# Kernel tuning notes

Hardware: AMD Instinct MI355X
Metric: run time of the kernel (lower is better)

Reference implementation:

```python
import jax, jax.numpy as jnp
import numpy as np

MAX_ITER = 20
F_TOL = 1e-6
FREE_NUM = 64  # free_idx[1] + 1
TRUNC = (0, 512)  # truncate_idx


def setup_inputs() -> dict:
    key = jax.random.key(0)
    ks = jax.random.split(key, 8)
    bsz, in_dim, hid, out_dim, m = 1024, 512, 1024, 256, 128
    return {
        "b_primal": jax.random.normal(ks[0], (bsz, in_dim), jnp.float32),
        "W0": jax.random.normal(ks[1], (hid, in_dim), jnp.float32) / np.sqrt(in_dim).astype(np.float32),
        "b0": jnp.zeros((hid,), jnp.float32),
        "W1": jax.random.normal(ks[2], (hid, hid), jnp.float32) / np.sqrt(hid).astype(np.float32),
        "b1": jnp.zeros((hid,), jnp.float32),
        "W2": jax.random.normal(ks[3], (out_dim, hid), jnp.float32) / np.sqrt(hid).astype(np.float32),
        "b2": jnp.zeros((out_dim,), jnp.float32),
        "A": jax.random.normal(ks[4], (m, out_dim), jnp.float32) * 0.1,
        "b_vec": jax.random.normal(ks[5], (m,), jnp.float32),
        # scaled so spectral norm < 1 -> contracting fixed-point iteration
        "WzProj": jax.random.normal(ks[6], (out_dim, out_dim), jnp.float32) * 0.03,
        "WbProj": jax.random.normal(ks[7], (out_dim, m), jnp.float32) * 0.1,
    }


def reference(b_primal, W0, b0, W1, b1, W2, b2, A, b_vec, WzProj, WbProj):
    # eval-mode forward of DualNN (report_projection=True)
    x = b_primal[:, TRUNC[0]:TRUNC[1]]
    h = jax.nn.relu(x @ W0.T + b0)
    h = jax.nn.relu(h @ W1.T + b1)
    out = h @ W2.T + b2                      # [bsz, output_dim]

    bias_proj = b_vec @ WbProj.T             # [output_dim]

    def cond(state):
        _, it, res = state
        return (it <= MAX_ITER) & (res > F_TOL)

    def body(state):
        z, it, _ = state
        z = bias_proj + z @ WzProj.T         # affine projection step
        u = z[:, :FREE_NUM]
        v = jax.nn.relu(z[:, FREE_NUM:])     # clamp non-free coordinates
        z = jnp.concatenate([u, v], axis=-1)
        res = jnp.max(jnp.abs(z @ A.T - b_vec))  # inf-norm equality residual
        return z, it + 1, res

    z_star, curr_iter, _ = jax.lax.while_loop(
        cond, body, (out, jnp.int32(1), jnp.float32(jnp.inf)))
    return (z_star, out, curr_iter)
```

## Files before the change

kernel.cpp:

```cpp
#include <hip/hip_runtime.h>

typedef __attribute__((ext_vector_type(8))) __bf16 bf16x8;
typedef __attribute__((ext_vector_type(4))) float f32x4;

#define MAX_ITER_N 20
#define F_TOL_F 1e-6f
#define FREE_NUM_N 64

#define BSZ 1024
#define IN_DIM 512
#define HID 1024
#define OUT_DIM 256
#define M_CON 128

#define WS_BAR   0
#define WS_RES   8
#define WS_BP    48
#define WS_H1    304
#define WS_H2    (WS_H1 + 524288)
#define WS_WZG   (WS_H2 + 524288)
#define WS_AG    (WS_WZG + 32768)

__device__ __forceinline__ unsigned short f2bf(float f) {
    unsigned int u = __float_as_uint(f);
    u += 0x7fffu + ((u >> 16) & 1u);
    return (unsigned short)(u >> 16);
}

__device__ __forceinline__ uint4 cvt8(float4 a, float4 b) {
    union { unsigned short s[8]; uint4 v; } u;
    u.s[0] = f2bf(a.x); u.s[1] = f2bf(a.y); u.s[2] = f2bf(a.z); u.s[3] = f2bf(a.w);
    u.s[4] = f2bf(b.x); u.s[5] = f2bf(b.y); u.s[6] = f2bf(b.z); u.s[7] = f2bf(b.w);
    return u.v;
}

__device__ __forceinline__ void gload_lds16(const unsigned short* g, unsigned short* l) {
    __builtin_amdgcn_global_load_lds(
        (const __attribute__((address_space(1))) unsigned int*)(const void*)g,
        (__attribute__((address_space(3))) unsigned int*)(void*)l, 16, 0, 0);
}

__device__ __forceinline__ bf16x8 ldfrag(const unsigned short* p) {
    return __builtin_bit_cast(bf16x8, *(const uint4*)p);
}

__device__ __forceinline__ bf16x8 frag128(const unsigned short* lds, int row, int gc) {
    int phys = gc ^ (row & 15);
    return __builtin_bit_cast(bf16x8, *(const uint4*)(lds + row * 128 + phys * 8));
}

__device__ __forceinline__ void grid_barrier(unsigned int* bar, unsigned int nblk) {
    __syncthreads();
    if (threadIdx.x == 0) {
        unsigned int g = __hip_atomic_load(&bar[1], __ATOMIC_RELAXED, __HIP_MEMORY_SCOPE_AGENT);
        unsigned int a = __hip_atomic_fetch_add(&bar[0], 1u, __ATOMIC_ACQ_REL, __HIP_MEMORY_SCOPE_AGENT);
        if (a == nblk - 1u) {
            __hip_atomic_store(&bar[0], 0u, __ATOMIC_RELAXED, __HIP_MEMORY_SCOPE_AGENT);
            __hip_atomic_store(&bar[1], g + 1u, __ATOMIC_RELEASE, __HIP_MEMORY_SCOPE_AGENT);
        } else {
            while (__hip_atomic_load(&bar[1], __ATOMIC_ACQUIRE, __HIP_MEMORY_SCOPE_AGENT) == g)
                __builtin_amdgcn_s_sleep(2);
        }
    }
    __syncthreads();
}

template<int K, int NTN, bool AF32, bool BF32, bool RELU, bool F32OUT>
__device__ __forceinline__ void gemm32_dev(
    const void* __restrict__ Av, const void* __restrict__ Bv,
    const float* __restrict__ bias, void* __restrict__ Cv, int N_,
    int tile, unsigned short (*As)[32 * 128], unsigned short (*Bs)[32 * 128])
{
    constexpr int NCH = K / 128;
    const int tid = threadIdx.x;
    const int w = tid >> 6;
    const int lane = tid & 63;
    const int ln = lane & 15;
    const int q  = lane >> 4;
    const int wr = w >> 1;
    const int wc = w & 1;
    const int row0 = (tile / NTN) * 32;
    const int col0 = (tile % NTN) * 32;

    int goff[2], lgran[2], soff[2], dbase[2];
#pragma unroll
    for (int i = 0; i < 2; ++i) {
        int P = i * 256 + tid;
        int row = P >> 4, gc = P & 15;
        goff[i]  = row * K + gc * 8;
        lgran[i] = row * 128 + (gc ^ (row & 15)) * 8;
        int base = w * 128 + i * 64;
        int P2 = base + lane;
        int row2 = P2 >> 4, pgc = P2 & 15;
        soff[i]  = row2 * K + (pgc ^ (row2 & 15)) * 8;
        dbase[i] = base * 8;
    }

    const float* Af = (const float*)Av + row0 * K;
    const float* Bf = (const float*)Bv + col0 * K;
    const unsigned short* Ah = (const unsigned short*)Av + row0 * K;
    const unsigned short* Bh = (const unsigned short*)Bv + col0 * K;

    float4 fa[2][2], fb[2][2];
    if constexpr (AF32) {
#pragma unroll
        for (int i = 0; i < 2; ++i) {
            fa[i][0] = *(const float4*)(Af + goff[i]);
            fa[i][1] = *(const float4*)(Af + goff[i] + 4);
        }
#pragma unroll
        for (int i = 0; i < 2; ++i) *(uint4*)&As[0][lgran[i]] = cvt8(fa[i][0], fa[i][1]);
    } else {
#pragma unroll
        for (int i = 0; i < 2; ++i) gload_lds16(Ah + soff[i], &As[0][dbase[i]]);
    }
    if constexpr (BF32) {
#pragma unroll
        for (int i = 0; i < 2; ++i) {
            fb[i][0] = *(const float4*)(Bf + goff[i]);
            fb[i][1] = *(const float4*)(Bf + goff[i] + 4);
        }
#pragma unroll
        for (int i = 0; i < 2; ++i) *(uint4*)&Bs[0][lgran[i]] = cvt8(fb[i][0], fb[i][1]);
    } else {
#pragma unroll
        for (int i = 0; i < 2; ++i) gload_lds16(Bh + soff[i], &Bs[0][dbase[i]]);
    }

    f32x4 acc = {0.f, 0.f, 0.f, 0.f};

    for (int c = 0; c < NCH; ++c) {
        __syncthreads();
        const int nb = (c + 1) & 1;
        if (c + 1 < NCH) {
            if constexpr (AF32) {
#pragma unroll
                for (int i = 0; i < 2; ++i) {
                    fa[i][0] = *(const float4*)(Af + (c + 1) * 128 + goff[i]);
                    fa[i][1] = *(const float4*)(Af + (c + 1) * 128 + goff[i] + 4);
                }
            } else {
#pragma unroll
                for (int i = 0; i < 2; ++i)
                    gload_lds16(Ah + (c + 1) * 128 + soff[i], &As[nb][dbase[i]]);
            }
            if constexpr (BF32) {
#pragma unroll
                for (int i = 0; i < 2; ++i) {
                    fb[i][0] = *(const float4*)(Bf + (c + 1) * 128 + goff[i]);
                    fb[i][1] = *(const float4*)(Bf + (c + 1) * 128 + goff[i] + 4);
                }
            } else {
#pragma unroll
                for (int i = 0; i < 2; ++i)
                    gload_lds16(Bh + (c + 1) * 128 + soff[i], &Bs[nb][dbase[i]]);
            }
        }
        const unsigned short* Ac = As[c & 1];
        const unsigned short* Bc = Bs[c & 1];
#pragma unroll
        for (int ks = 0; ks < 4; ++ks) {
            bf16x8 af = frag128(Ac, wr * 16 + ln, ks * 4 + q);
            bf16x8 bf = frag128(Bc, wc * 16 + ln, ks * 4 + q);
            acc = __builtin_amdgcn_mfma_f32_16x16x32_bf16(af, bf, acc, 0, 0, 0);
        }
        if (c + 1 < NCH) {
            if constexpr (AF32) {
#pragma unroll
                for (int i = 0; i < 2; ++i) *(uint4*)&As[nb][lgran[i]] = cvt8(fa[i][0], fa[i][1]);
            }
            if constexpr (BF32) {
#pragma unroll
                for (int i = 0; i < 2; ++i) *(uint4*)&Bs[nb][lgran[i]] = cvt8(fb[i][0], fb[i][1]);
            }
        }
    }

    const int cc = col0 + wc * 16 + ln;
    const float bv = bias[cc];
#pragma unroll
    for (int i = 0; i < 4; ++i) {
        int r = row0 + wr * 16 + q * 4 + i;
        float v = acc[i] + bv;
        if (RELU) v = fmaxf(v, 0.0f);
        if (F32OUT) ((float*)Cv)[r * N_ + cc] = v;
        else ((unsigned short*)Cv)[r * N_ + cc] = f2bf(v);
    }
}

__global__ __launch_bounds__(256, 4) void g1_k(
    const float* __restrict__ b_primal, const float* __restrict__ W0,
    const float* __restrict__ b0, float* __restrict__ ws)
{
    __shared__ __align__(16) unsigned short As[2][32 * 128];
    __shared__ __align__(16) unsigned short Bs[2][32 * 128];
    if (blockIdx.x == 0 && threadIdx.x < 40)
        ((unsigned int*)ws)[threadIdx.x] = 0u;
    unsigned short* h1c = (unsigned short*)(ws + WS_H1);
    gemm32_dev<IN_DIM, 32, true, true, true, false>(b_primal, W0, b0, h1c, HID,
                                                    blockIdx.x, As, Bs);
}

__global__ __launch_bounds__(256, 4) void g2_k(
    const float* __restrict__ W1, const float* __restrict__ b1,
    const float* __restrict__ Wz, const float* __restrict__ Amat,
    const float* __restrict__ b_vec, const float* __restrict__ WbProj,
    float* __restrict__ ws)
{
    __shared__ __align__(16) unsigned short As[2][32 * 128];
    __shared__ __align__(16) unsigned short Bs[2][32 * 128];
    const int tid = threadIdx.x;
    if (blockIdx.x >= 1024) {
        int b = blockIdx.x - 1024;
        if (b == 96) {
            float s = 0.0f;
            const float* wrow = WbProj + tid * M_CON;
            for (int k = 0; k < M_CON; ++k) s += b_vec[k] * wrow[k];
            (ws + WS_BP)[tid] = s;
            return;
        }
        const float* src; unsigned short* dst; int off;
        if (b < 64) { src = Wz;   dst = (unsigned short*)(ws + WS_WZG); off = b; }
        else        { src = Amat; dst = (unsigned short*)(ws + WS_AG);  off = b - 64; }
        int idx = off * 1024 + tid * 4;
        float4 v = *(const float4*)(src + idx);
        ushort4 o;
        o.x = f2bf(v.x); o.y = f2bf(v.y); o.z = f2bf(v.z); o.w = f2bf(v.w);
        *(ushort4*)(dst + idx) = o;
        return;
    }
    const unsigned short* h1c = (const unsigned short*)(ws + WS_H1);
    unsigned short* h2c = (unsigned short*)(ws + WS_H2);
    gemm32_dev<HID, 32, false, true, true, false>(h1c, W1, b1, h2c, HID,
                                                  blockIdx.x, As, Bs);
}

__global__ __launch_bounds__(256, 4) void g3_k(
    const float* __restrict__ W2, const float* __restrict__ b2,
    float* __restrict__ out, float* __restrict__ ws)
{
    __shared__ __align__(16) unsigned short As[2][32 * 128];
    __shared__ __align__(16) unsigned short Bs[2][32 * 128];
    const unsigned short* h2c = (const unsigned short*)(ws + WS_H2);
    float* outz = out + BSZ * OUT_DIM;
    gemm32_dev<HID, 8, false, true, false, true>(h2c, W2, b2, outz, OUT_DIM,
                                                 blockIdx.x, As, Bs);
}

__global__ __launch_bounds__(256, 1) void loop_k(
    const float* __restrict__ b_vec, const float* __restrict__ WzProj,
    float* __restrict__ out, float* __restrict__ ws)
{
    __shared__ __align__(16) unsigned char smem[16 * 257 * 4 + 64];
    unsigned int* bar = (unsigned int*)(ws + WS_BAR);
    unsigned int* res = (unsigned int*)(ws + WS_RES);
    const float* bp = ws + WS_BP;
    const unsigned short* WzG = (const unsigned short*)(ws + WS_WZG);
    const unsigned short* AG  = (const unsigned short*)(ws + WS_AG);
    float* outz = out + BSZ * OUT_DIM;

    const int tid  = threadIdx.x;
    const int wave = tid >> 6;
    const int lane = tid & 63;
    const int ln   = lane & 15;
    const int q    = lane >> 4;
    const int r0   = blockIdx.x * 16;

    unsigned short (*zS)[264] = (unsigned short(*)[264])smem;
    float* red = (float*)(smem + 16 * 257 * 4);

    {
        int row = tid >> 4;
        int c0  = (tid & 15) * 16;
        const float* src = outz + (r0 + row) * OUT_DIM + c0;
#pragma unroll
        for (int i = 0; i < 16; ++i) zS[row][c0 + i] = f2bf(src[i]);
    }

    bf16x8 afr[2][8];
    float bvv[2];
#pragma unroll
    for (int mt = 0; mt < 2; ++mt) {
        int m = wave * 32 + mt * 16 + ln;
        bvv[mt] = b_vec[m];
#pragma unroll
        for (int ks = 0; ks < 8; ++ks)
            afr[mt][ks] = ldfrag(AG + m * OUT_DIM + ks * 32 + q * 8);
    }
    int colg[4];
    float bpv[4];
    bf16x8 wzfr[4][8];
#pragma unroll
    for (int nt = 0; nt < 4; ++nt) {
        colg[nt] = wave * 64 + nt * 16 + ln;
        bpv[nt]  = bp[colg[nt]];
#pragma unroll
        for (int ks = 0; ks < 8; ++ks)
            wzfr[nt][ks] = ldfrag(WzG + colg[nt] * OUT_DIM + ks * 32 + q * 8);
    }
    __syncthreads();

    bf16x8 zfr[8];
#pragma unroll
    for (int ks = 0; ks < 8; ++ks)
        zfr[ks] = __builtin_bit_cast(bf16x8, *(const uint4*)&zS[ln][ks * 32 + q * 8]);

    const f32x4 zero4 = {0.f, 0.f, 0.f, 0.f};

    for (int t = 1; t <= MAX_ITER_N; ++t) {
        f32x4 acc[4];
#pragma unroll
        for (int nt = 0; nt < 4; ++nt) acc[nt] = zero4;
#pragma unroll
        for (int ks = 0; ks < 8; ++ks)
#pragma unroll
            for (int nt = 0; nt < 4; ++nt)
                acc[nt] = __builtin_amdgcn_mfma_f32_16x16x32_bf16(zfr[ks], wzfr[nt][ks], acc[nt], 0, 0, 0);
        float vals[4][4];
#pragma unroll
        for (int nt = 0; nt < 4; ++nt)
#pragma unroll
            for (int i = 0; i < 4; ++i) {
                float v = acc[nt][i] + bpv[nt];
                if (colg[nt] >= FREE_NUM_N) v = fmaxf(v, 0.0f);
                vals[nt][i] = v;
            }
        if (t == MAX_ITER_N) {
#pragma unroll
            for (int nt = 0; nt < 4; ++nt)
#pragma unroll
                for (int i = 0; i < 4; ++i)
                    out[(r0 + q * 4 + i) * OUT_DIM + colg[nt]] = vals[nt][i];
        }
        __syncthreads();
#pragma unroll
        for (int nt = 0; nt < 4; ++nt)
#pragma unroll
            for (int i = 0; i < 4; ++i)
                zS[q * 4 + i][colg[nt]] = f2bf(vals[nt][i]);
        __syncthreads();
#pragma unroll
        for (int ks = 0; ks < 8; ++ks)
            zfr[ks] = __builtin_bit_cast(bf16x8, *(const uint4*)&zS[ln][ks * 32 + q * 8]);

        f32x4 acc2[2];
        acc2[0] = zero4; acc2[1] = zero4;
#pragma unroll
        for (int ks = 0; ks < 8; ++ks)
#pragma unroll
            for (int mt = 0; mt < 2; ++mt)
                acc2[mt] = __builtin_amdgcn_mfma_f32_16x16x32_bf16(zfr[ks], afr[mt][ks], acc2[mt], 0, 0, 0);
        float lmax = 0.0f;
#pragma unroll
        for (int mt = 0; mt < 2; ++mt)
#pragma unroll
            for (int i = 0; i < 4; ++i)
                lmax = fmaxf(lmax, fabsf(acc2[mt][i] - bvv[mt]));
#pragma unroll
        for (int off = 32; off > 0; off >>= 1)
            lmax = fmaxf(lmax, __shfl_xor(lmax, off));
        if (lane == 0) red[wave] = lmax;
        __syncthreads();
        if (tid == 0) {
            float bm = fmaxf(fmaxf(red[0], red[1]), fmaxf(red[2], red[3]));
            atomicMax(res + (t - 1), __float_as_uint(bm));
        }
    }

    grid_barrier(bar, 64);

    int T = MAX_ITER_N;
    for (int t = 0; t < MAX_ITER_N; ++t) {
        float r = __uint_as_float(res[t]);
        if (!(r > F_TOL_F)) { T = t + 1; break; }
    }
    if (blockIdx.x == 0 && tid == 0)
        out[2 * BSZ * OUT_DIM] = (float)(T + 1);

    if (T < MAX_ITER_N) {
        float (*zF)[257] = (float(*)[257])smem;
        const int row = tid >> 4;
        const int c0 = (tid & 15) * 16;
        __syncthreads();
        for (int i = 0; i < 16; ++i) zF[row][c0 + i] = outz[(r0 + row) * OUT_DIM + c0 + i];
        __syncthreads();
        const int j = tid;
        const float bj = bp[j];
        for (int t = 0; t < T; ++t) {
            float acc[16] = {};
            for (int k = 0; k < OUT_DIM; ++k) {
                float w = WzProj[j * OUT_DIM + k];
#pragma unroll
                for (int r = 0; r < 16; ++r) acc[r] += zF[r][k] * w;
            }
            __syncthreads();
#pragma unroll
            for (int r = 0; r < 16; ++r) {
                float v = acc[r] + bj;
                if (j >= FREE_NUM_N) v = fmaxf(v, 0.0f);
                zF[r][j] = v;
            }
            __syncthreads();
        }
        for (int i = 0; i < 16; ++i) out[(r0 + row) * OUT_DIM + c0 + i] = zF[row][c0 + i];
    }
}

extern "C" void kernel_launch(void* const* d_in, const int* in_sizes, int n_in,
                              void* d_out, int out_size, void* d_ws, size_t ws_size,
                              hipStream_t stream) {
    const float* b_primal = (const float*)d_in[0];
    const float* W0     = (const float*)d_in[1];
    const float* b0     = (const float*)d_in[2];
    const float* W1     = (const float*)d_in[3];
    const float* b1     = (const float*)d_in[4];
    const float* W2     = (const float*)d_in[5];
    const float* b2     = (const float*)d_in[6];
    const float* Amat   = (const float*)d_in[7];
    const float* b_vec  = (const float*)d_in[8];
    const float* WzProj = (const float*)d_in[9];
    const float* WbProj = (const float*)d_in[10];
    float* out = (float*)d_out;
    float* ws  = (float*)d_ws;

    hipLaunchKernelGGL(g1_k, dim3(1024), dim3(256), 0, stream,
                       b_primal, W0, b0, ws);
    hipLaunchKernelGGL(g2_k, dim3(1024 + 97), dim3(256), 0, stream,
                       W1, b1, WzProj, Amat, b_vec, WbProj, ws);
    hipLaunchKernelGGL(g3_k, dim3(256), dim3(256), 0, stream,
                       W2, b2, out, ws);
    hipLaunchKernelGGL(loop_k, dim3(64), dim3(256), 0, stream,
                       b_vec, WzProj, out, ws);
}
```

Baseline: 144.3 us.

## Split-K the final GEMM, fuse partial reduction into loop kernel, shorten MFMA chains

```diff
diff --git a/kernel.cpp b/kernel.cpp
--- a/kernel.cpp
+++ b/kernel.cpp
@@ -20,6 +20,7 @@
 #define WS_H2    (WS_H1 + 524288)
 #define WS_WZG   (WS_H2 + 524288)
 #define WS_AG    (WS_WZG + 32768)
+#define WS_P0    (WS_AG + 16384)
 
 __device__ __forceinline__ unsigned short f2bf(float f) {
     unsigned int u = __float_as_uint(f);
@@ -65,13 +66,14 @@
     __syncthreads();
 }
 
-template<int K, int NTN, bool AF32, bool BF32, bool RELU, bool F32OUT>
+template<int Kext, bool AF32, bool BF32, bool RELU, int OUTMODE>
 __device__ __forceinline__ void gemm32_dev(
     const void* __restrict__ Av, const void* __restrict__ Bv,
     const float* __restrict__ bias, void* __restrict__ Cv, int N_,
-    int tile, unsigned short (*As)[32 * 128], unsigned short (*Bs)[32 * 128])
+    int ldA, int ldB, int tile, int NTN,
+    unsigned short (*As)[32 * 128], unsigned short (*Bs)[32 * 128])
 {
-    constexpr int NCH = K / 128;
+    constexpr int NCH = Kext / 128;
     const int tid = threadIdx.x;
     const int w = tid >> 6;
     const int lane = tid & 63;
@@ -82,49 +84,51 @@
     const int row0 = (tile / NTN) * 32;
     const int col0 = (tile % NTN) * 32;
 
-    int goff[2], lgran[2], soff[2], dbase[2];
+    int goffA[2], goffB[2], lgran[2], soffA[2], soffB[2], dbase[2];
 #pragma unroll
     for (int i = 0; i < 2; ++i) {
         int P = i * 256 + tid;
         int row = P >> 4, gc = P & 15;
-        goff[i]  = row * K + gc * 8;
+        goffA[i] = row * ldA + gc * 8;
+        goffB[i] = row * ldB + gc * 8;
         lgran[i] = row * 128 + (gc ^ (row & 15)) * 8;
         int base = w * 128 + i * 64;
         int P2 = base + lane;
-        int row2 = P2 >> 4, pgc = P2 & 15;
-        soff[i]  = row2 * K + (pgc ^ (row2 & 15)) * 8;
+        int row2 = P2 >> 4, pgc = (P2 & 15) ^ (row2 & 15);
+        soffA[i] = row2 * ldA + pgc * 8;
+        soffB[i] = row2 * ldB + pgc * 8;
         dbase[i] = base * 8;
     }
 
-    const float* Af = (const float*)Av + row0 * K;
-    const float* Bf = (const float*)Bv + col0 * K;
-    const unsigned short* Ah = (const unsigned short*)Av + row0 * K;
-    const unsigned short* Bh = (const unsigned short*)Bv + col0 * K;
+    const float* Af = (const float*)Av;
+    const float* Bf = (const float*)Bv;
+    const unsigned short* Ah = (const unsigned short*)Av;
+    const unsigned short* Bh = (const unsigned short*)Bv;
 
     float4 fa[2][2], fb[2][2];
     if constexpr (AF32) {
 #pragma unroll
         for (int i = 0; i < 2; ++i) {
-            fa[i][0] = *(const float4*)(Af + goff[i]);
-            fa[i][1] = *(const float4*)(Af + goff[i] + 4);
+            fa[i][0] = *(const float4*)(Af + goffA[i]);
+            fa[i][1] = *(const float4*)(Af + goffA[i] + 4);
         }
 #pragma unroll
         for (int i = 0; i < 2; ++i) *(uint4*)&As[0][lgran[i]] = cvt8(fa[i][0], fa[i][1]);
     } else {
 #pragma unroll
-        for (int i = 0; i < 2; ++i) gload_lds16(Ah + soff[i], &As[0][dbase[i]]);
+        for (int i = 0; i < 2; ++i) gload_lds16(Ah + soffA[i], &As[0][dbase[i]]);
     }
     if constexpr (BF32) {
 #pragma unroll
         for (int i = 0; i < 2; ++i) {
-            fb[i][0] = *(const float4*)(Bf + goff[i]);
-            fb[i][1] = *(const float4*)(Bf + goff[i] + 4);
+            fb[i][0] = *(const float4*)(Bf + goffB[i]);
+            fb[i][1] = *(const float4*)(Bf + goffB[i] + 4);
         }
 #pragma unroll
         for (int i = 0; i < 2; ++i) *(uint4*)&Bs[0][lgran[i]] = cvt8(fb[i][0], fb[i][1]);
     } else {
 #pragma unroll
-        for (int i = 0; i < 2; ++i) gload_lds16(Bh + soff[i], &Bs[0][dbase[i]]);
+        for (int i = 0; i < 2; ++i) gload_lds16(Bh + soffB[i], &Bs[0][dbase[i]]);
     }
 
     f32x4 acc = {0.f, 0.f, 0.f, 0.f};
@@ -136,24 +140,24 @@
             if constexpr (AF32) {
 #pragma unroll
                 for (int i = 0; i < 2; ++i) {
-                    fa[i][0] = *(const float4*)(Af + (c + 1) * 128 + goff[i]);
-                    fa[i][1] = *(const float4*)(Af + (c + 1) * 128 + goff[i] + 4);
+                    fa[i][0] = *(const float4*)(Af + (c + 1) * 128 + goffA[i]);
+                    fa[i][1] = *(const float4*)(Af + (c + 1) * 128 + goffA[i] + 4);
                 }
             } else {
 #pragma unroll
                 for (int i = 0; i < 2; ++i)
-                    gload_lds16(Ah + (c + 1) * 128 + soff[i], &As[nb][dbase[i]]);
+                    gload_lds16(Ah + (c + 1) * 128 + soffA[i], &As[nb][dbase[i]]);
             }
             if constexpr (BF32) {
 #pragma unroll
                 for (int i = 0; i < 2; ++i) {
-                    fb[i][0] = *(const float4*)(Bf + (c + 1) * 128 + goff[i]);
-                    fb[i][1] = *(const float4*)(Bf + (c + 1) * 128 + goff[i] + 4);
+                    fb[i][0] = *(const float4*)(Bf + (c + 1) * 128 + goffB[i]);
+                    fb[i][1] = *(const float4*)(Bf + (c + 1) * 128 + goffB[i] + 4);
                 }
             } else {
 #pragma unroll
                 for (int i = 0; i < 2; ++i)
-                    gload_lds16(Bh + (c + 1) * 128 + soff[i], &Bs[nb][dbase[i]]);
+                    gload_lds16(Bh + (c + 1) * 128 + soffB[i], &Bs[nb][dbase[i]]);
             }
         }
         const unsigned short* Ac = As[c & 1];
@@ -177,18 +181,25 @@
     }
 
     const int cc = col0 + wc * 16 + ln;
-    const float bv = bias[cc];
-#pragma unroll
-    for (int i = 0; i < 4; ++i) {
-        int r = row0 + wr * 16 + q * 4 + i;
-        float v = acc[i] + bv;
-        if (RELU) v = fmaxf(v, 0.0f);
-        if (F32OUT) ((float*)Cv)[r * N_ + cc] = v;
-        else ((unsigned short*)Cv)[r * N_ + cc] = f2bf(v);
-    }
-}
-
-__global__ __launch_bounds__(256, 4) void g1_k(
+    if constexpr (OUTMODE == 0) {
+        const float bv = bias[cc];
+#pragma unroll
+        for (int i = 0; i < 4; ++i) {
+            int r = row0 + wr * 16 + q * 4 + i;
+            float v = acc[i] + bv;
+            if (RELU) v = fmaxf(v, 0.0f);
+            ((unsigned short*)Cv)[r * N_ + cc] = f2bf(v);
+        }
+    } else {
+#pragma unroll
+        for (int i = 0; i < 4; ++i) {
+            int r = row0 + wr * 16 + q * 4 + i;
+            ((float*)Cv)[r * N_ + cc] = acc[i];
+        }
+    }
+}
+
+__global__ __launch_bounds__(256, 5) void g1_k(
     const float* __restrict__ b_primal, const float* __restrict__ W0,
     const float* __restrict__ b0, float* __restrict__ ws)
 {
@@ -197,11 +208,14 @@
     if (blockIdx.x == 0 && threadIdx.x < 40)
         ((unsigned int*)ws)[threadIdx.x] = 0u;
     unsigned short* h1c = (unsigned short*)(ws + WS_H1);
-    gemm32_dev<IN_DIM, 32, true, true, true, false>(b_primal, W0, b0, h1c, HID,
-                                                    blockIdx.x, As, Bs);
-}
-
-__global__ __launch_bounds__(256, 4) void g2_k(
+    const int tile = blockIdx.x;
+    const float* Ab = b_primal + (tile / 32) * 32 * IN_DIM;
+    const float* Bb = W0 + (tile % 32) * 32 * IN_DIM;
+    gemm32_dev<IN_DIM, true, true, true, 0>(Ab, Bb, b0, h1c, HID,
+                                            IN_DIM, IN_DIM, tile, 32, As, Bs);
+}
+
+__global__ __launch_bounds__(256, 5) void g2_k(
     const float* __restrict__ W1, const float* __restrict__ b1,
     const float* __restrict__ Wz, const float* __restrict__ Amat,
     const float* __restrict__ b_vec, const float* __restrict__ WbProj,
@@ -231,25 +245,32 @@
     }
     const unsigned short* h1c = (const unsigned short*)(ws + WS_H1);
     unsigned short* h2c = (unsigned short*)(ws + WS_H2);
-    gemm32_dev<HID, 32, false, true, true, false>(h1c, W1, b1, h2c, HID,
-                                                  blockIdx.x, As, Bs);
+    const int tile = blockIdx.x;
+    const unsigned short* Ab = h1c + (tile / 32) * 32 * HID;
+    const float* Bb = W1 + (tile % 32) * 32 * HID;
+    gemm32_dev<HID, false, true, true, 0>(Ab, Bb, b1, h2c, HID,
+                                          HID, HID, tile, 32, As, Bs);
 }
 
 __global__ __launch_bounds__(256, 4) void g3_k(
-    const float* __restrict__ W2, const float* __restrict__ b2,
-    float* __restrict__ out, float* __restrict__ ws)
+    const float* __restrict__ W2, float* __restrict__ ws)
 {
     __shared__ __align__(16) unsigned short As[2][32 * 128];
     __shared__ __align__(16) unsigned short Bs[2][32 * 128];
     const unsigned short* h2c = (const unsigned short*)(ws + WS_H2);
-    float* outz = out + BSZ * OUT_DIM;
-    gemm32_dev<HID, 8, false, true, false, true>(h2c, W2, b2, outz, OUT_DIM,
-                                                 blockIdx.x, As, Bs);
+    const int tile = blockIdx.x & 255;
+    const int half = blockIdx.x >> 8;
+    float* part = ws + WS_P0 + half * (BSZ * OUT_DIM);
+    const unsigned short* Ab = h2c + (tile / 8) * 32 * HID + half * 512;
+    const float* Bb = W2 + (tile % 8) * 32 * HID + half * 512;
+    gemm32_dev<512, false, true, false, 1>(Ab, Bb, nullptr, part, OUT_DIM,
+                                           HID, HID, tile, 8, As, Bs);
 }
 
 __global__ __launch_bounds__(256, 1) void loop_k(
-    const float* __restrict__ b_vec, const float* __restrict__ WzProj,
-    float* __restrict__ out, float* __restrict__ ws)
+    const float* __restrict__ b2, const float* __restrict__ b_vec,
+    const float* __restrict__ WzProj, float* __restrict__ out,
+    float* __restrict__ ws)
 {
     __shared__ __align__(16) unsigned char smem[16 * 257 * 4 + 64];
     unsigned int* bar = (unsigned int*)(ws + WS_BAR);
@@ -257,6 +278,8 @@
     const float* bp = ws + WS_BP;
     const unsigned short* WzG = (const unsigned short*)(ws + WS_WZG);
     const unsigned short* AG  = (const unsigned short*)(ws + WS_AG);
+    const float* p0 = ws + WS_P0;
+    const float* p1 = ws + WS_P0 + BSZ * OUT_DIM;
     float* outz = out + BSZ * OUT_DIM;
 
     const int tid  = threadIdx.x;
@@ -267,14 +290,25 @@
     const int r0   = blockIdx.x * 16;
 
     unsigned short (*zS)[264] = (unsigned short(*)[264])smem;
-    float* red = (float*)(smem + 16 * 257 * 4);
 
     {
         int row = tid >> 4;
         int c0  = (tid & 15) * 16;
-        const float* src = outz + (r0 + row) * OUT_DIM + c0;
-#pragma unroll
-        for (int i = 0; i < 16; ++i) zS[row][c0 + i] = f2bf(src[i]);
+        int base = (r0 + row) * OUT_DIM + c0;
+#pragma unroll
+        for (int v4 = 0; v4 < 4; ++v4) {
+            float4 a = *(const float4*)(p0 + base + v4 * 4);
+            float4 b = *(const float4*)(p1 + base + v4 * 4);
+            float4 bb = *(const float4*)(b2 + c0 + v4 * 4);
+            float4 o;
+            o.x = a.x + b.x + bb.x; o.y = a.y + b.y + bb.y;
+            o.z = a.z + b.z + bb.z; o.w = a.w + b.w + bb.w;
+            *(float4*)(outz + base + v4 * 4) = o;
+            zS[row][c0 + v4 * 4 + 0] = f2bf(o.x);
+            zS[row][c0 + v4 * 4 + 1] = f2bf(o.y);
+            zS[row][c0 + v4 * 4 + 2] = f2bf(o.z);
+            zS[row][c0 + v4 * 4 + 3] = f2bf(o.w);
+        }
     }
 
     bf16x8 afr[2][8];
@@ -308,20 +342,22 @@
     const f32x4 zero4 = {0.f, 0.f, 0.f, 0.f};
 
     for (int t = 1; t <= MAX_ITER_N; ++t) {
-        f32x4 acc[4];
-#pragma unroll
-        for (int nt = 0; nt < 4; ++nt) acc[nt] = zero4;
-#pragma unroll
-        for (int ks = 0; ks < 8; ++ks)
-#pragma unroll
-            for (int nt = 0; nt < 4; ++nt)
-                acc[nt] = __builtin_amdgcn_mfma_f32_16x16x32_bf16(zfr[ks], wzfr[nt][ks], acc[nt], 0, 0, 0);
+        f32x4 accA[4], accB[4];
+#pragma unroll
+        for (int nt = 0; nt < 4; ++nt) { accA[nt] = zero4; accB[nt] = zero4; }
+#pragma unroll
+        for (int ks = 0; ks < 4; ++ks)
+#pragma unroll
+            for (int nt = 0; nt < 4; ++nt) {
+                accA[nt] = __builtin_amdgcn_mfma_f32_16x16x32_bf16(zfr[ks], wzfr[nt][ks], accA[nt], 0, 0, 0);
+                accB[nt] = __builtin_amdgcn_mfma_f32_16x16x32_bf16(zfr[ks + 4], wzfr[nt][ks + 4], accB[nt], 0, 0, 0);
+            }
         float vals[4][4];
 #pragma unroll
         for (int nt = 0; nt < 4; ++nt)
 #pragma unroll
             for (int i = 0; i < 4; ++i) {
-                float v = acc[nt][i] + bpv[nt];
+                float v = accA[nt][i] + accB[nt][i] + bpv[nt];
                 if (colg[nt] >= FREE_NUM_N) v = fmaxf(v, 0.0f);
                 vals[nt][i] = v;
             }
@@ -343,28 +379,26 @@
         for (int ks = 0; ks < 8; ++ks)
             zfr[ks] = __builtin_bit_cast(bf16x8, *(const uint4*)&zS[ln][ks * 32 + q * 8]);
 
-        f32x4 acc2[2];
-        acc2[0] = zero4; acc2[1] = zero4;
-#pragma unroll
-        for (int ks = 0; ks < 8; ++ks)
-#pragma unroll
-            for (int mt = 0; mt < 2; ++mt)
-                acc2[mt] = __builtin_amdgcn_mfma_f32_16x16x32_bf16(zfr[ks], afr[mt][ks], acc2[mt], 0, 0, 0);
+        f32x4 r2A[2], r2B[2];
+        r2A[0] = zero4; r2A[1] = zero4; r2B[0] = zero4; r2B[1] = zero4;
+#pragma unroll
+        for (int ks = 0; ks < 4; ++ks)
+#pragma unroll
+            for (int mt = 0; mt < 2; ++mt) {
+                r2A[mt] = __builtin_amdgcn_mfma_f32_16x16x32_bf16(zfr[ks], afr[mt][ks], r2A[mt], 0, 0, 0);
+                r2B[mt] = __builtin_amdgcn_mfma_f32_16x16x32_bf16(zfr[ks + 4], afr[mt][ks + 4], r2B[mt], 0, 0, 0);
+            }
         float lmax = 0.0f;
 #pragma unroll
         for (int mt = 0; mt < 2; ++mt)
 #pragma unroll
             for (int i = 0; i < 4; ++i)
-                lmax = fmaxf(lmax, fabsf(acc2[mt][i] - bvv[mt]));
+                lmax = fmaxf(lmax, fabsf(r2A[mt][i] + r2B[mt][i] - bvv[mt]));
 #pragma unroll
         for (int off = 32; off > 0; off >>= 1)
             lmax = fmaxf(lmax, __shfl_xor(lmax, off));
-        if (lane == 0) red[wave] = lmax;
-        __syncthreads();
-        if (tid == 0) {
-            float bm = fmaxf(fmaxf(red[0], red[1]), fmaxf(red[2], red[3]));
-            atomicMax(res + (t - 1), __float_as_uint(bm));
-        }
+        if (lane == 0)
+            atomicMax(res + (t - 1), __float_as_uint(lmax));
     }
 
     grid_barrier(bar, 64);
@@ -427,8 +461,8 @@
                        b_primal, W0, b0, ws);
     hipLaunchKernelGGL(g2_k, dim3(1024 + 97), dim3(256), 0, stream,
                        W1, b1, WzProj, Amat, b_vec, WbProj, ws);
-    hipLaunchKernelGGL(g3_k, dim3(256), dim3(256), 0, stream,
-                       W2, b2, out, ws);
+    hipLaunchKernelGGL(g3_k, dim3(512), dim3(256), 0, stream,
+                       W2, ws);
     hipLaunchKernelGGL(loop_k, dim3(64), dim3(256), 0, stream,
-                       b_vec, WzProj, out, ws);
-}
+                       b2, b_vec, WzProj, out, ws);
+}
```

Measured after the change: 175.6 us. 21.7% more time.
